# Performance work log

Hardware: AMD Instinct MI355X
Metric: run time of the kernel (lower is better)

## Reference

```python
import jax, jax.numpy as jnp
import numpy as np

B, H, W = 64, 14, 14
DIM, NH, LORA = 768, 12, 4
HD = DIM // NH  # 64


def setup_inputs() -> dict:
    key = jax.random.key(0)
    ks = jax.random.split(key, 12)
    s = 0.02
    return {
        "x": jax.random.normal(ks[0], (B, H, W, DIM), dtype=jnp.float32),
        "qkv_w": jax.random.normal(ks[1], (3 * DIM, DIM), dtype=jnp.float32) * s,
        "qkv_b": jax.random.normal(ks[2], (3 * DIM,), dtype=jnp.float32) * s,
        "proj_w": jax.random.normal(ks[3], (DIM, DIM), dtype=jnp.float32) * s,
        "proj_b": jax.random.normal(ks[4], (DIM,), dtype=jnp.float32) * s,
        "la_q": jax.random.normal(ks[5], (LORA, DIM), dtype=jnp.float32) * s,
        "lb_q": jax.random.normal(ks[6], (DIM, LORA), dtype=jnp.float32) * s,
        "la_v": jax.random.normal(ks[7], (LORA, DIM), dtype=jnp.float32) * s,
        "lb_v": jax.random.normal(ks[8], (DIM, LORA), dtype=jnp.float32) * s,
        "rel_pos_h": jax.random.normal(ks[9], (2 * H - 1, HD), dtype=jnp.float32) * s,
        "rel_pos_w": jax.random.normal(ks[10], (2 * W - 1, HD), dtype=jnp.float32) * s,
    }


def reference(x, qkv_w, qkv_b, proj_w, proj_b, la_q, lb_q, la_v, lb_v, rel_pos_h, rel_pos_w):
    b, h, w, c = x.shape
    nh, hd = NH, c // NH
    scale = hd ** -0.5

    # qkv projection with LoRA deltas on q and v
    qkv = x @ qkv_w.T + qkv_b                       # (b,h,w,3c)
    new_q = (x @ la_q.T) @ lb_q.T                   # (b,h,w,c)
    new_v = (x @ la_v.T) @ lb_v.T
    qkv = qkv.at[..., :c].add(new_q)
    qkv = qkv.at[..., 2 * c:].add(new_v)

    qkv = qkv.reshape(b, h * w, 3, nh, hd).transpose(2, 0, 3, 1, 4)
    qkv = qkv.reshape(3, b * nh, h * w, hd)
    q, k, v = qkv[0], qkv[1], qkv[2]

    attn = jnp.einsum('bqd,bkd->bqk', q * scale, k)  # (b*nh, hw, hw)

    # decomposed relative position bias; q_size == k_size so no interpolation
    idx_h = jnp.arange(h)[:, None] - jnp.arange(h)[None, :] + (h - 1)
    idx_w = jnp.arange(w)[:, None] - jnp.arange(w)[None, :] + (w - 1)
    Rh = rel_pos_h[idx_h]                            # (h,h,hd)
    Rw = rel_pos_w[idx_w]                            # (w,w,hd)
    r_q = q.reshape(b * nh, h, w, hd)
    rel_h = jnp.einsum('bhwc,hkc->bhwk', r_q, Rh)    # (b*nh,h,w,h)
    rel_w = jnp.einsum('bhwc,wkc->bhwk', r_q, Rw)    # (b*nh,h,w,w)
    attn = (attn.reshape(b * nh, h, w, h, w)
            + rel_h[:, :, :, :, None]
            + rel_w[:, :, :, None, :]).reshape(b * nh, h * w, h * w)

    attn = jax.nn.softmax(attn, axis=-1)
    out = jnp.einsum('bqk,bkd->bqd', attn, v)        # (b*nh, hw, hd)
    out = out.reshape(b, nh, h, w, hd).transpose(0, 2, 3, 1, 4).reshape(b, h, w, c)
    return out @ proj_w.T + proj_b
```

## Files before the change

kernel.cpp:

```cpp
#include <hip/hip_runtime.h>
#include <stdint.h>

#define DIM   768
#define NH    12
#define HD    64
#define NT    196
#define M_ROWS 12544

typedef __attribute__((ext_vector_type(8))) short bf16x8;
typedef __attribute__((ext_vector_type(4))) float f32x4;

__device__ __forceinline__ float b2f(short s) {
  union { unsigned u; float f; } c;
  c.u = ((unsigned)(unsigned short)s) << 16;
  return c.f;
}
__device__ __forceinline__ short f2b(float f) {
  union { float f; unsigned u; } c; c.f = f;
  unsigned u = c.u;
  u += 0x7fffu + ((u >> 16) & 1u);
  return (short)(u >> 16);
}

__device__ __forceinline__ f32x4 mfma16(bf16x8 a, bf16x8 b, f32x4 c) {
  return __builtin_amdgcn_mfma_f32_16x16x32_bf16(a, b, c, 0, 0, 0);
}

__device__ __forceinline__ void g2lds16(const short* g, short* l) {
  __builtin_amdgcn_global_load_lds(
      (const __attribute__((address_space(1))) void*)g,
      (__attribute__((address_space(3))) void*)l, 16, 0, 0);
}

struct CvtArgs { const float* src[4]; int n4[4]; int off[4]; };

__global__ __launch_bounds__(256) void k_cvt(CvtArgs a, short* __restrict__ dst) {
  const int tid = blockIdx.x * 256 + threadIdx.x;
  const int stride = gridDim.x * 256;
  #pragma unroll
  for (int s = 0; s < 4; ++s) {
    const float4* sp = (const float4*)a.src[s];
    short4* dp = (short4*)(dst + a.off[s]);
    const int n4 = a.n4[s];
    for (int i = tid; i < n4; i += stride) {
      float4 v = sp[i];
      short4 o = { f2b(v.x), f2b(v.y), f2b(v.z), f2b(v.w) };
      dp[i] = o;
    }
  }
}

__global__ __launch_bounds__(256) void k_lora_xa(
    const float* __restrict__ x, const float* __restrict__ la_q,
    const float* __restrict__ la_v, float* __restrict__ xa,
    short* __restrict__ xb)
{
  __shared__ float sla[8][DIM];
  const int tid = threadIdx.x;
  for (int i = tid; i < 8 * DIM; i += 256) {
    int j = i / DIM, c = i - j * DIM;
    sla[j][c] = (j < 4) ? la_q[j * DIM + c] : la_v[(j - 4) * DIM + c];
  }
  __syncthreads();
  const int lane = tid & 63, wid = tid >> 6;
  const int m = blockIdx.x * 4 + wid;
  const float4* xr = (const float4*)(x + (size_t)m * DIM);
  short4* xbr = (short4*)(xb + (size_t)m * DIM);
  float s[8] = {};
  #pragma unroll
  for (int i = 0; i < 3; ++i) {
    float4 xv = xr[lane + 64 * i];
    short4 o = { f2b(xv.x), f2b(xv.y), f2b(xv.z), f2b(xv.w) };
    xbr[lane + 64 * i] = o;
    int c = (lane + 64 * i) * 4;
    #pragma unroll
    for (int j = 0; j < 8; ++j)
      s[j] += xv.x * sla[j][c] + xv.y * sla[j][c + 1]
            + xv.z * sla[j][c + 2] + xv.w * sla[j][c + 3];
  }
  #pragma unroll
  for (int j = 0; j < 8; ++j) {
    #pragma unroll
    for (int off = 32; off; off >>= 1) s[j] += __shfl_xor(s[j], off);
  }
  if (lane == 0) {
    float* o = xa + m * 8;
    #pragma unroll
    for (int j = 0; j < 8; ++j) o[j] = s[j];
  }
}

template<int EPI, int NCOL>
__global__ __launch_bounds__(512) void k_gemm2(
    const short* __restrict__ A, const short* __restrict__ B,
    const float* __restrict__ bias, const float* __restrict__ xa,
    const float* __restrict__ lb_q, const float* __restrict__ lb_v,
    short* __restrict__ out, float* __restrict__ outf)
{
  constexpr int K = DIM;
  constexpr int NWG = 49 * NCOL;
  constexpr int Qc = NWG / 8, Rc = NWG % 8;
  extern __shared__ short smem[];

  const int g = blockIdx.x;
  const int xcd = g & 7, idx = g >> 3;
  const int wgid = (xcd < Rc) ? xcd * (Qc + 1) + idx
                              : Rc * (Qc + 1) + (xcd - Rc) * Qc + idx;
  const int rm0 = (wgid / NCOL) * 256;
  const int cn0 = (wgid % NCOL) * 256;

  const int tid = threadIdx.x, lane = tid & 63, wid = tid >> 6;
  const int wm = (wid >> 2) * 128, wn = (wid & 3) * 64;
  const int fr = lane & 15, fg = lane >> 4;
  f32x4 acc[8][4] = {};

  const int srow = tid >> 2;
  const int spos = ((tid & 3) ^ ((tid >> 3) & 3)) * 8;
  const short* gaT = A + (size_t)(rm0 + srow) * K + spos;
  const short* gbT = B + (size_t)(cn0 + srow) * K + spos;
  const int swz8 = (fg ^ ((fr >> 1) & 3)) * 8;

#define STG(buf, T, s)                                                      \
  do {                                                                      \
    const short* g0 = ((s) & 1) ? gbT : gaT;                                \
    short* d0 = smem + (buf) * 32768 + ((s) & 1) * 16384                    \
                + ((s) >> 1) * 8192 + tid * 8;                              \
    g2lds16(g0 + (T) * 64 + ((s) >> 1) * 32, d0);                           \
    g2lds16(g0 + (size_t)128 * K + (T) * 64 + ((s) >> 1) * 32, d0 + 4096);  \
  } while (0)

  STG(0, 0, 0); STG(0, 0, 1); STG(0, 0, 2); STG(0, 0, 3);
  asm volatile("s_waitcnt vmcnt(0)" ::: "memory");
  __builtin_amdgcn_s_barrier();
  __builtin_amdgcn_sched_barrier(0);

  bf16x8 af[8];
  for (int T = 0; T < 12; ++T) {
    const int b = T & 1;
    const short* pA = smem + b * 32768;
    const short* pB = pA + 16384;
    #pragma unroll
    for (int q = 0; q < 4; ++q) {
      const int kh = q >> 1, jh = q & 1;
      if (jh == 0) {
        #pragma unroll
        for (int i = 0; i < 8; ++i)
          af[i] = *(const bf16x8*)&pA[kh * 8192 + (wm + i * 16 + fr) * 32 + swz8];
      }
      bf16x8 bg0 = *(const bf16x8*)&pB[kh * 8192 + (wn + (jh * 2 + 0) * 16 + fr) * 32 + swz8];
      bf16x8 bg1 = *(const bf16x8*)&pB[kh * 8192 + (wn + (jh * 2 + 1) * 16 + fr) * 32 + swz8];
      if (T + 1 < 12) {
        STG(b ^ 1, T + 1, q);
        asm volatile("s_waitcnt vmcnt(4)" ::: "memory");
      } else {
        asm volatile("s_waitcnt vmcnt(0)" ::: "memory");
      }
      __builtin_amdgcn_s_barrier();
      asm volatile("s_waitcnt lgkmcnt(0)" ::: "memory");
      __builtin_amdgcn_sched_barrier(0);
      __builtin_amdgcn_s_setprio(1);
      #pragma unroll
      for (int i = 0; i < 8; ++i) {
        acc[i][jh * 2 + 0] = mfma16(af[i], bg0, acc[i][jh * 2 + 0]);
        acc[i][jh * 2 + 1] = mfma16(af[i], bg1, acc[i][jh * 2 + 1]);
      }
      __builtin_amdgcn_s_setprio(0);
      __builtin_amdgcn_s_barrier();
    }
  }
#undef STG

  int ncol[4]; float biasv[4];
  #pragma unroll
  for (int j = 0; j < 4; ++j) {
    ncol[j] = cn0 + wn + j * 16 + fr;
    biasv[j] = bias[ncol[j]];
  }

  if (EPI == 0) {
    const int reg = cn0 / DIM;
    float lb[4][4];
    if (reg != 1) {
      const float* lbt = (reg == 0) ? lb_q : lb_v;
      #pragma unroll
      for (int j = 0; j < 4; ++j) {
        int ni = ncol[j] - reg * DIM;
        #pragma unroll
        for (int l = 0; l < 4; ++l) lb[j][l] = lbt[ni * 4 + l];
      }
    }
    #pragma unroll
    for (int i = 0; i < 8; ++i) {
      #pragma unroll
      for (int r = 0; r < 4; ++r) {
        int m = rm0 + wm + i * 16 + fg * 4 + r;
        int b_i = m / NT, p = m - b_i * NT;
        float xv0 = 0, xv1 = 0, xv2 = 0, xv3 = 0;
        if (reg != 1) {
          const float* xp = xa + m * 8 + (reg == 2 ? 4 : 0);
          xv0 = xp[0]; xv1 = xp[1]; xv2 = xp[2]; xv3 = xp[3];
        }
        #pragma unroll
        for (int j = 0; j < 4; ++j) {
          float val = acc[i][j][r] + biasv[j];
          if (reg != 1)
            val += xv0 * lb[j][0] + xv1 * lb[j][1] + xv2 * lb[j][2] + xv3 * lb[j][3];
          int ni = ncol[j] - reg * DIM;
          int head = ni >> 6, d = ni & 63;
          out[(size_t)reg * (M_ROWS * DIM)
              + ((size_t)(b_i * NH + head) * NT + p) * HD + d] = f2b(val);
        }
      }
    }
  } else {
    #pragma unroll
    for (int i = 0; i < 8; ++i)
      #pragma unroll
      for (int r = 0; r < 4; ++r) {
        int m = rm0 + wm + i * 16 + fg * 4 + r;
        #pragma unroll
        for (int j = 0; j < 4; ++j)
          outf[(size_t)m * DIM + ncol[j]] = acc[i][j][r] + biasv[j];
      }
  }
}

__global__ __launch_bounds__(256) void k_attn(
    const short* __restrict__ qb, const short* __restrict__ kb,
    const short* __restrict__ vb, const short* __restrict__ rph,
    const short* __restrict__ rpw, short* __restrict__ ao)
{
  __shared__ short vst[64 * 256];
  __shared__ short kst[NT * 64];
  __shared__ short pwb[4 * 16 * 72];
  __shared__ short relh[NT * 14];
  __shared__ short relw[NT * 14];
  const int tid = threadIdx.x, lane = tid & 63, wid = tid >> 6;
  const int fr = lane & 15, fg = lane >> 4;
  const int bh = blockIdx.x;
  const int b_i = bh / NH, head = bh - b_i * NH;
  const short* q0 = qb + (size_t)bh * NT * HD;
  const short* k0 = kb + (size_t)bh * NT * HD;
  const short* v0 = vb + (size_t)bh * NT * HD;

  for (int t = tid; t < NT * 8; t += 256) {
    int row = t >> 3, slot = t & 7;
    g2lds16(k0 + row * 64 + ((slot ^ (row & 7)) * 8), &kst[t * 8]);
  }

  for (int i = tid; i < 64 * 12; i += 256) {
    int row = i / 12, c = 196 + (i - (i / 12) * 12);
    vst[row * 256 + (c ^ (((row >> 2) & 7) * 8))] = 0;
  }
  for (int t = tid; t < NT * 8; t += 256) {
    int p = t >> 3, d0 = (t & 7) * 8;
    bf16x8 vv = *(const bf16x8*)(v0 + p * HD + d0);
    #pragma unroll
    for (int j = 0; j < 8; ++j)
      vst[(d0 + j) * 256 + (p ^ ((((d0 + j) >> 2) & 7) * 8))] = vv[j];
  }
  for (int job = wid; job < 28; job += 4) {
    const int isW = job >= 14 ? 1 : 0;
    const int fx = isW ? job - 14 : job;
    const int qrow = isW ? fr * 14 + fx : fx * 14 + fr;
    const bool aok = fr < 14;
    const short* rp = isW ? rpw : rph;
    int ridx = fx - fr + 13;
    ridx = ridx < 0 ? 0 : (ridx > 26 ? 26 : ridx);
    f32x4 racc = {0.f, 0.f, 0.f, 0.f};
    #pragma unroll
    for (int ks = 0; ks < 2; ++ks) {
      bf16x8 afr = {0,0,0,0,0,0,0,0};
      if (aok) afr = *(const bf16x8*)(q0 + qrow * HD + ks * 32 + fg * 8);
      bf16x8 bfr = *(const bf16x8*)(rp + ridx * HD + ks * 32 + fg * 8);
      racc = mfma16(afr, bfr, racc);
    }
    #pragma unroll
    for (int r = 0; r < 4; ++r) {
      int rr = fg * 4 + r;
      if (rr < 14 && fr < 14) {
        int p = isW ? rr * 14 + fx : fx * 14 + rr;
        (isW ? relw : relh)[p * 14 + fr] = f2b(racc[r]);
      }
    }
  }
  __syncthreads();

  const float scale = 0.125f;
  const int p0 = fg ^ (fr & 7);
  const int p1 = (fg + 4) ^ (fr & 7);
  for (int t = wid; t < 13; t += 4) {
    const int m0 = t * 16;
    bf16x8 aq0 = {0,0,0,0,0,0,0,0}, aq1 = {0,0,0,0,0,0,0,0};
    {
      int arow = m0 + fr;
      if (arow < NT) {
        aq0 = *(const bf16x8*)(q0 + arow * HD + fg * 8);
        aq1 = *(const bf16x8*)(q0 + arow * HD + 32 + fg * 8);
      }
    }
    f32x4 sc[13] = {};
    #pragma unroll
    for (int ct = 0; ct < 13; ++ct) {
      int brow = ct * 16 + fr;
      bf16x8 bk0 = {0,0,0,0,0,0,0,0}, bk1 = {0,0,0,0,0,0,0,0};
      if (brow < NT) {
        bk0 = *(const bf16x8*)&kst[brow * 64 + p0 * 8];
        bk1 = *(const bf16x8*)&kst[brow * 64 + p1 * 8];
      }
      sc[ct] = mfma16(aq0, bk0, sc[ct]);
      sc[ct] = mfma16(aq1, bk1, sc[ct]);
    }
    float rsum[4] = {0.f, 0.f, 0.f, 0.f};
    #pragma unroll
    for (int ct = 0; ct < 13; ++ct) {
      int kk = ct * 16 + fr;
      int kh = kk / 14, kw = kk - kh * 14;
      #pragma unroll
      for (int r = 0; r < 4; ++r) {
        int p = m0 + fg * 4 + r;
        float e;
        if (kk < NT && p < NT)
          e = __expf(sc[ct][r] * scale + b2f(relh[p * 14 + kh])
                     + b2f(relw[p * 14 + kw]));
        else
          e = 0.f;
        sc[ct][r] = e;
        rsum[r] += e;
      }
    }
    #pragma unroll
    for (int r = 0; r < 4; ++r) {
      rsum[r] += __shfl_xor(rsum[r], 1);
      rsum[r] += __shfl_xor(rsum[r], 2);
      rsum[r] += __shfl_xor(rsum[r], 4);
      rsum[r] += __shfl_xor(rsum[r], 8);
    }

    f32x4 oacc[4] = {};
    #pragma unroll
    for (int qd = 0; qd < 4; ++qd) {
      const int ctb = qd * 4;
      const int nct = (qd == 3) ? 1 : 4;
      #pragma unroll
      for (int cl = 0; cl < 4; ++cl) {
        if (cl < nct) {
          #pragma unroll
          for (int r = 0; r < 4; ++r)
            pwb[(wid * 16 + fg * 4 + r) * 72 + cl * 16 + fr] =
                f2b(sc[ctb + cl][r]);
        }
      }
      const int nks = (qd == 3) ? 1 : 2;
      #pragma unroll
      for (int ks = 0; ks < 2; ++ks) {
        if (ks < nks) {
          const bool hi = (qd == 3) && (fg >= 2);
          bf16x8 pa = {0,0,0,0,0,0,0,0};
          if (!hi) pa = *(const bf16x8*)&pwb[(wid * 16 + fr) * 72 + ks * 32 + fg * 8];
          const int c = qd * 64 + ks * 32 + fg * 8;
          #pragma unroll
          for (int dt = 0; dt < 4; ++dt) {
            bf16x8 vv = {0,0,0,0,0,0,0,0};
            if (!hi)
              vv = *(const bf16x8*)&vst[(fr * 4 + dt) * 256 + (c ^ ((fr & 7) * 8))];
            oacc[dt] = mfma16(pa, vv, oacc[dt]);
          }
        }
      }
    }
    #pragma unroll
    for (int r = 0; r < 4; ++r) {
      int p = m0 + fg * 4 + r;
      if (p < NT) {
        float inv = 1.0f / rsum[r];
        size_t base = ((size_t)(b_i * NT + p)) * DIM + head * HD + fr * 4;
        short4 o4 = { f2b(oacc[0][r] * inv), f2b(oacc[1][r] * inv),
                      f2b(oacc[2][r] * inv), f2b(oacc[3][r] * inv) };
        *(short4*)&ao[base] = o4;
      }
    }
  }
}

extern "C" void kernel_launch(void* const* d_in, const int* in_sizes, int n_in,
                              void* d_out, int out_size, void* d_ws, size_t ws_size,
                              hipStream_t stream) {
  const float *x = nullptr, *qkv_w = nullptr, *qkv_b = nullptr,
              *proj_w = nullptr, *proj_b = nullptr, *rph = nullptr,
              *rpw = nullptr;
  const float* c3072[4] = {nullptr, nullptr, nullptr, nullptr};
  int n3072 = 0, n1728 = 0;
  for (int i = 0; i < n_in; ++i) {
    const float* p = (const float*)d_in[i];
    switch (in_sizes[i]) {
      case 9633792: x = p; break;
      case 1769472: qkv_w = p; break;
      case 2304:    qkv_b = p; break;
      case 589824:  proj_w = p; break;
      case 768:     proj_b = p; break;
      case 3072:    if (n3072 < 4) c3072[n3072++] = p; break;
      case 1728:    { if (n1728 == 0) rph = p; else rpw = p; ++n1728; } break;
      default: break;
    }
  }
  const bool alpha = (n_in >= 1 && in_sizes[n_in - 1] == 9633792);
  const float* la_q = c3072[0];
  const float* lb_q = alpha ? c3072[2] : c3072[1];
  const float* la_v = alpha ? c3072[1] : c3072[2];
  const float* lb_v = c3072[3];

  float* out = (float*)d_out;

  char* ws = (char*)d_ws;
  float* xa   = (float*)ws;
  short* qkvb = (short*)(ws + 401408);
  short* q_   = qkvb;
  short* k_   = qkvb + (size_t)M_ROWS * DIM;
  short* v_   = qkvb + (size_t)2 * M_ROWS * DIM;
  short* cvt  = (short*)(ws + 401408 + 57802752);
  short* xb      = cvt;
  short* qkv_wb  = cvt + 9633792;
  short* proj_wb = cvt + 11403264;
  short* rphb    = cvt + 11993088;
  short* rpwb    = cvt + 11994816;
  short* ao = xb;

  CvtArgs ca;
  ca.src[0] = qkv_w;  ca.n4[0] = 1769472 / 4;  ca.off[0] = 9633792;
  ca.src[1] = proj_w; ca.n4[1] =  589824 / 4;  ca.off[1] = 11403264;
  ca.src[2] = rph;    ca.n4[2] =    1728 / 4;  ca.off[2] = 11993088;
  ca.src[3] = rpw;    ca.n4[3] =    1728 / 4;  ca.off[3] = 11994816;

  hipFuncSetAttribute((const void*)k_gemm2<0, 9>,
                      hipFuncAttributeMaxDynamicSharedMemorySize, 131072);
  hipFuncSetAttribute((const void*)k_gemm2<1, 3>,
                      hipFuncAttributeMaxDynamicSharedMemorySize, 131072);

  k_cvt<<<512, 256, 0, stream>>>(ca, cvt);
  k_lora_xa<<<3136, 256, 0, stream>>>(x, la_q, la_v, xa, xb);
  k_gemm2<0, 9><<<441, 512, 131072, stream>>>(xb, qkv_wb, qkv_b, xa, lb_q,
                                              lb_v, qkvb, nullptr);
  k_attn<<<768, 256, 0, stream>>>(q_, k_, v_, rphb, rpwb, ao);
  k_gemm2<1, 3><<<147, 512, 131072, stream>>>(ao, proj_wb, proj_b, nullptr,
                                              nullptr, nullptr, nullptr, out);
}
```

Measured before the change: 181.7 us.

## Shrink GEMM K-tile to 32 with static LDS double buffer, simpler pipeline

The GEMM main loop now uses a K-tile of 32 over 24 iterations instead of 64 split into four sub-stages over 12 iterations. Each stage loads all A and B fragments and then issues the full 8x4 MFMA block, with one barrier pair per tile. LDS drops from 128 KB of dynamic shared memory to 64 KB of static arrays, which could allow more resident workgroups per CU. The cost is twice as many barriers and global-to-LDS waits, and less fine-grained overlap of the prefetch with the MFMAs.

```diff
diff --git a/kernel.cpp b/kernel.cpp
--- a/kernel.cpp
+++ b/kernel.cpp
@@ -100,7 +100,8 @@
   constexpr int K = DIM;
   constexpr int NWG = 49 * NCOL;
   constexpr int Qc = NWG / 8, Rc = NWG % 8;
-  extern __shared__ short smem[];
+  __shared__ short sA[2 * 8192];
+  __shared__ short sB[2 * 8192];
 
   const int g = blockIdx.x;
   const int xcd = g & 7, idx = g >> 3;
@@ -115,58 +116,53 @@
   f32x4 acc[8][4] = {};
 
   const int srow = tid >> 2;
-  const int spos = ((tid & 3) ^ ((tid >> 3) & 3)) * 8;
-  const short* gaT = A + (size_t)(rm0 + srow) * K + spos;
-  const short* gbT = B + (size_t)(cn0 + srow) * K + spos;
+  const int slot8 = ((tid & 3) ^ ((tid >> 3) & 3)) * 8;
+  const short* gaT = A + (size_t)(rm0 + srow) * K + slot8;
+  const short* gbT = B + (size_t)(cn0 + srow) * K + slot8;
+  short* dA = sA + tid * 8;
+  short* dB = sB + tid * 8;
   const int swz8 = (fg ^ ((fr >> 1) & 3)) * 8;
 
-#define STG(buf, T, s)                                                      \
-  do {                                                                      \
-    const short* g0 = ((s) & 1) ? gbT : gaT;                                \
-    short* d0 = smem + (buf) * 32768 + ((s) & 1) * 16384                    \
-                + ((s) >> 1) * 8192 + tid * 8;                              \
-    g2lds16(g0 + (T) * 64 + ((s) >> 1) * 32, d0);                           \
-    g2lds16(g0 + (size_t)128 * K + (T) * 64 + ((s) >> 1) * 32, d0 + 4096);  \
+#define STG(buf, T)                                                   \
+  do {                                                                \
+    g2lds16(gaT + (T) * 32,                    dA + (buf) * 8192);    \
+    g2lds16(gaT + (size_t)128 * K + (T) * 32,  dA + (buf) * 8192 + 4096); \
+    g2lds16(gbT + (T) * 32,                    dB + (buf) * 8192);    \
+    g2lds16(gbT + (size_t)128 * K + (T) * 32,  dB + (buf) * 8192 + 4096); \
   } while (0)
 
-  STG(0, 0, 0); STG(0, 0, 1); STG(0, 0, 2); STG(0, 0, 3);
+  STG(0, 0);
   asm volatile("s_waitcnt vmcnt(0)" ::: "memory");
   __builtin_amdgcn_s_barrier();
   __builtin_amdgcn_sched_barrier(0);
 
-  bf16x8 af[8];
-  for (int T = 0; T < 12; ++T) {
+  for (int T = 0; T < 24; ++T) {
     const int b = T & 1;
-    const short* pA = smem + b * 32768;
-    const short* pB = pA + 16384;
-    #pragma unroll
-    for (int q = 0; q < 4; ++q) {
-      const int kh = q >> 1, jh = q & 1;
-      if (jh == 0) {
-        #pragma unroll
-        for (int i = 0; i < 8; ++i)
-          af[i] = *(const bf16x8*)&pA[kh * 8192 + (wm + i * 16 + fr) * 32 + swz8];
-      }
-      bf16x8 bg0 = *(const bf16x8*)&pB[kh * 8192 + (wn + (jh * 2 + 0) * 16 + fr) * 32 + swz8];
-      bf16x8 bg1 = *(const bf16x8*)&pB[kh * 8192 + (wn + (jh * 2 + 1) * 16 + fr) * 32 + swz8];
-      if (T + 1 < 12) {
-        STG(b ^ 1, T + 1, q);
-        asm volatile("s_waitcnt vmcnt(4)" ::: "memory");
-      } else {
-        asm volatile("s_waitcnt vmcnt(0)" ::: "memory");
-      }
-      __builtin_amdgcn_s_barrier();
-      asm volatile("s_waitcnt lgkmcnt(0)" ::: "memory");
-      __builtin_amdgcn_sched_barrier(0);
-      __builtin_amdgcn_s_setprio(1);
-      #pragma unroll
-      for (int i = 0; i < 8; ++i) {
-        acc[i][jh * 2 + 0] = mfma16(af[i], bg0, acc[i][jh * 2 + 0]);
-        acc[i][jh * 2 + 1] = mfma16(af[i], bg1, acc[i][jh * 2 + 1]);
-      }
-      __builtin_amdgcn_s_setprio(0);
-      __builtin_amdgcn_s_barrier();
-    }
+    if (T + 1 < 24) {
+      STG(b ^ 1, T + 1);
+      asm volatile("s_waitcnt vmcnt(4)" ::: "memory");
+    } else {
+      asm volatile("s_waitcnt vmcnt(0)" ::: "memory");
+    }
+    __builtin_amdgcn_s_barrier();
+    __builtin_amdgcn_sched_barrier(0);
+    const short* pA = sA + b * 8192;
+    const short* pB = sB + b * 8192;
+    bf16x8 af[8], bg[4];
+    #pragma unroll
+    for (int i = 0; i < 8; ++i)
+      af[i] = *(const bf16x8*)&pA[(wm + i * 16 + fr) * 32 + swz8];
+    #pragma unroll
+    for (int j = 0; j < 4; ++j)
+      bg[j] = *(const bf16x8*)&pB[(wn + j * 16 + fr) * 32 + swz8];
+    __builtin_amdgcn_s_setprio(1);
+    #pragma unroll
+    for (int i = 0; i < 8; ++i)
+      #pragma unroll
+      for (int j = 0; j < 4; ++j)
+        acc[i][j] = mfma16(af[i], bg[j], acc[i][j]);
+    __builtin_amdgcn_s_setprio(0);
+    __builtin_amdgcn_s_barrier();
   }
 #undef STG
 
@@ -432,16 +428,11 @@
   ca.src[2] = rph;    ca.n4[2] =    1728 / 4;  ca.off[2] = 11993088;
   ca.src[3] = rpw;    ca.n4[3] =    1728 / 4;  ca.off[3] = 11994816;
 
-  hipFuncSetAttribute((const void*)k_gemm2<0, 9>,
-                      hipFuncAttributeMaxDynamicSharedMemorySize, 131072);
-  hipFuncSetAttribute((const void*)k_gemm2<1, 3>,
-                      hipFuncAttributeMaxDynamicSharedMemorySize, 131072);
-
   k_cvt<<<512, 256, 0, stream>>>(ca, cvt);
   k_lora_xa<<<3136, 256, 0, stream>>>(x, la_q, la_v, xa, xb);
-  k_gemm2<0, 9><<<441, 512, 131072, stream>>>(xb, qkv_wb, qkv_b, xa, lb_q,
-                                              lb_v, qkvb, nullptr);
+  k_gemm2<0, 9><<<441, 512, 0, stream>>>(xb, qkv_wb, qkv_b, xa, lb_q,
+                                         lb_v, qkvb, nullptr);
   k_attn<<<768, 256, 0, stream>>>(q_, k_, v_, rphb, rpwb, ao);
-  k_gemm2<1, 3><<<147, 512, 131072, stream>>>(ao, proj_wb, proj_b, nullptr,
-                                              nullptr, nullptr, nullptr, out);
-}
+  k_gemm2<1, 3><<<147, 512, 0, stream>>>(ao, proj_wb, proj_b, nullptr,
+                                         nullptr, nullptr, nullptr, out);
+}
```

Result: slower. 204.8 us (+12.7%).
